# Optimization experiments

Hardware: AMD Instinct MI355X
Metric: run time of the kernel (lower is better)

Reference implementation:

```python
import jax, jax.numpy as jnp
import numpy as np
from jax.ops import segment_sum, segment_max

E = 300000
H = 256
NC = 20000
EPS = 1e-6
RESIDUAL_UNIFORM = 0.2


def setup_inputs() -> dict:
    key = jax.random.key(0)
    k = jax.random.split(key, 6)
    edge_repr = jax.random.normal(k[0], (E, H), dtype=jnp.float32)
    edge_weight = jax.random.uniform(k[1], (E,), dtype=jnp.float32)
    case_idx = jax.random.randint(k[2], (E,), 0, NC)
    W1 = jax.random.normal(k[3], (4 * H, H), dtype=jnp.float32) * (1.0 / np.sqrt(4 * H))
    b1 = jnp.zeros((H,), dtype=jnp.float32)
    W2 = jax.random.normal(k[4], (H, 1), dtype=jnp.float32) * (1.0 / np.sqrt(H))
    b2 = jnp.zeros((1,), dtype=jnp.float32)
    return {"edge_repr": edge_repr, "edge_weight": edge_weight, "case_idx": case_idx,
            "num_case": NC, "W1": W1, "b1": b1, "W2": W2, "b2": b2}


def reference(edge_repr, edge_weight, case_idx, num_case, W1, b1, W2, b2):
    # --- leave-one-out context per edge ---
    weighted = edge_repr * edge_weight[:, None]                       # [E,H]
    case_deg = segment_sum(edge_weight, case_idx, num_segments=num_case)   # [NC]
    case_sum = segment_sum(weighted, case_idx, num_segments=num_case)      # [NC,H]
    base_case_repr = case_sum / jnp.maximum(case_deg, EPS)[:, None]        # [NC,H]

    edge_case_deg = case_deg[case_idx][:, None]                       # [E,1]
    w2d = edge_weight[:, None]
    remaining = edge_case_deg - w2d
    ctx_loocv = (case_sum[case_idx] - weighted) / jnp.maximum(remaining, 1e-8)
    fallback = (remaining <= EPS).astype(edge_repr.dtype)
    ctx = fallback * base_case_repr[case_idx] + (1.0 - fallback) * ctx_loocv  # [E,H]

    # --- attention MLP on [e, ctx, e*ctx, |e-ctx|] ---
    feat = jnp.concatenate([edge_repr, ctx, edge_repr * ctx,
                            jnp.abs(edge_repr - ctx)], axis=-1)       # [E,4H]
    h = jax.nn.relu(feat @ W1 + b1)                                   # [E,H] (dropout = identity in eval)
    logits = (h @ W2 + b2)[:, 0]                                      # [E]

    # --- grouped (per-case) stable softmax ---
    gmax = segment_max(logits, case_idx, num_segments=num_case)
    gmax = jnp.where(jnp.isneginf(gmax), jnp.zeros_like(gmax), gmax)
    exp_val = jnp.exp(logits - gmax[case_idx])
    gsum = segment_sum(exp_val, case_idx, num_segments=num_case)
    alpha = exp_val / (gsum[case_idx] + 1e-8)

    uniform_alpha = edge_weight / (case_deg[case_idx] + 1e-8)
    final_alpha = (1.0 - RESIDUAL_UNIFORM) * alpha + RESIDUAL_UNIFORM * uniform_alpha

    case_repr = segment_sum(final_alpha[:, None] * edge_repr, case_idx,
                            num_segments=num_case)                    # [NC,H]
    return case_repr
```

## Files before the change

### kernel.cpp

```cpp
#include <hip/hip_runtime.h>
#include <hip/hip_bf16.h>
#include <math.h>

#define H 256
#define EPSV 1e-6f

typedef __attribute__((ext_vector_type(8))) short bf16x8;
typedef __attribute__((ext_vector_type(4))) float f32x4;
typedef __attribute__((ext_vector_type(4))) unsigned int uint4v;

static __device__ __forceinline__ unsigned short f2bf(float x){
  union { float f; unsigned u; } v; v.f = x;
  unsigned r = v.u + 0x7FFF + ((v.u >> 16) & 1);
  return (unsigned short)(r >> 16);
}
static __device__ __forceinline__ unsigned pk2(unsigned short lo, unsigned short hi){
  return (unsigned)lo | ((unsigned)hi << 16);
}

__global__ void count_kernel(const int* __restrict__ cidx, int* __restrict__ counts, int E){
  int e = blockIdx.x * blockDim.x + threadIdx.x;
  if (e < E) atomicAdd(&counts[cidx[e]], 1);
}

__global__ __launch_bounds__(1024) void scan_offsets(const int* __restrict__ counts,
                                                     int* __restrict__ offsets, int n){
  __shared__ int a[1024];
  int tid = threadIdx.x;
  int per = (n + 1023) >> 10;
  int start = tid * per;
  int end = min(start + per, n);
  int s = 0;
  for (int i = start; i < end; ++i) s += counts[i];
  a[tid] = s;
  __syncthreads();
  for (int d = 1; d < 1024; d <<= 1){
    int v = 0;
    if (tid >= d) v = a[tid - d];
    __syncthreads();
    if (tid >= d) a[tid] += v;
    __syncthreads();
  }
  int run = a[tid] - s;
  for (int i = start; i < end; ++i){ offsets[i] = run; run += counts[i]; }
  if (tid == 1023) offsets[n] = a[1023];
}

__global__ void fill_kernel(const int* __restrict__ cidx, int* __restrict__ cursor,
                            const int* __restrict__ offs, int* __restrict__ elist, int E){
  int e = blockIdx.x * blockDim.x + threadIdx.x;
  if (e < E){
    int c = cidx[e];
    int pos = atomicAdd(&cursor[c], 1);
    elist[offs[c] + pos] = e;
  }
}

__global__ __launch_bounds__(64) void sort_lists(int* __restrict__ elist,
                                                 const int* __restrict__ offs, int nc){
  int c = blockIdx.x, lane = threadIdx.x;
  int s = offs[c], e = offs[c + 1];
  int n = e - s;
  if (n <= 1) return;
  __shared__ int vals[128];
  if (n <= 128){
    int v0 = (lane < n)      ? elist[s + lane]      : 0;
    int v1 = (64 + lane < n) ? elist[s + 64 + lane] : 0;
    vals[lane] = v0; vals[64 + lane] = v1;
    __syncthreads();
    int r0 = 0, r1 = 0;
    for (int j = 0; j < n; ++j){
      int vj = vals[j];
      r0 += (vj < v0); r1 += (vj < v1);
    }
    if (lane < n)      elist[s + r0] = v0;
    if (64 + lane < n) elist[s + r1] = v1;
  } else if (lane == 0){
    for (int i = s + 1; i < e; ++i){
      int v = elist[i];
      int j = i - 1;
      while (j >= s && elist[j] > v){ elist[j + 1] = elist[j]; --j; }
      elist[j + 1] = v;
    }
  }
}

__global__ void w1_convert(const float* __restrict__ W1, unsigned short* __restrict__ w1t2s){
  int t = blockIdx.x * blockDim.x + threadIdx.x;
  int k = t >> 8, n = t & 255;
  int kg = k >> 5, klo = k & 31;
  unsigned b = (unsigned)((n & 63) * 64 + klo * 2);
  b ^= ((b >> 7) & 3u) << 4;
  size_t byteaddr = (size_t)kg * 16384 + (size_t)(n >> 6) * 4096 + b;
  w1t2s[byteaddr >> 1] = f2bf(W1[t]);
}

__global__ __launch_bounds__(64) void case_sums(const float* __restrict__ er,
                                                const float* __restrict__ ew,
                                                const int* __restrict__ elist,
                                                const int* __restrict__ offs,
                                                float* __restrict__ csum,
                                                float* __restrict__ cdeg){
  int c = blockIdx.x, lane = threadIdx.x;
  int s = offs[c], e = offs[c + 1];
  f32x4 acc = (f32x4){0.f,0.f,0.f,0.f};
  float dacc = 0.f;
  int i = s;
  for (; i + 1 < e; i += 2){
    int e1 = elist[i], e2 = elist[i + 1];
    float w1 = ew[e1], w2 = ew[e2];
    f32x4 v1 = *(const f32x4*)&er[(size_t)e1 * H + lane * 4];
    f32x4 v2 = *(const f32x4*)&er[(size_t)e2 * H + lane * 4];
    acc += v1 * w1;
    acc += v2 * w2;
    dacc += w1; dacc += w2;
  }
  if (i < e){
    int e1 = elist[i];
    float w1 = ew[e1];
    acc += (*(const f32x4*)&er[(size_t)e1 * H + lane * 4]) * w1;
    dacc += w1;
  }
  *(f32x4*)&csum[(size_t)c * H + lane * 4] = acc;
  if (lane == 0) cdeg[c] = dacc;
}

__global__ __launch_bounds__(256, 2) void fused_mlp(
    const float* __restrict__ er, const float* __restrict__ ew,
    const int* __restrict__ cidx, const float* __restrict__ cdeg,
    const float* __restrict__ csum, const unsigned short* __restrict__ w1t2s,
    const float* __restrict__ b1, const float* __restrict__ w2,
    const float* __restrict__ b2, float* __restrict__ logits, int E)
{
  __shared__ __align__(16) unsigned short featl[4 * 2048];
  __shared__ __align__(16) unsigned short Bst[2 * 8192];
  __shared__ float lpart[4][64];
  int tid = threadIdx.x;
  long e0 = (long)blockIdx.x * 64;

  int wn = tid >> 6, lane = tid & 63;
  int l15 = lane & 15, lg = lane >> 4;

  int r = tid >> 2, q = tid & 3;
  long e = e0 + r;
  bool valid = (e < (long)E);
  long ec = valid ? e : 0;
  int   cce = cidx[ec];
  float w   = valid ? ew[ec] : 0.f;
  float deg = valid ? cdeg[cce] : 1.f;
  float rem = deg - w;
  bool  fb  = (rem <= EPSV);
  float inv  = fb ? (1.0f / fmaxf(deg, EPSV)) : (1.0f / fmaxf(rem, 1e-8f));
  float wsel = fb ? 0.f : w;
  float vm   = valid ? 1.f : 0.f;
  const float* erow = er   + (size_t)ec  * H + q * 8;
  const float* srow = csum + (size_t)cce * H + q * 8;
  unsigned packoff = (unsigned)r * 32u + ((unsigned)(q ^ ((r >> 1) & 3))) * 8u;

  f32x4 acc[4][4];
  #pragma unroll
  for (int mt = 0; mt < 4; ++mt)
    #pragma unroll
    for (int nt = 0; nt < 4; ++nt) acc[mt][nt] = (f32x4){0.f,0.f,0.f,0.f};

  f32x4 xr[2], sr[2];

#define LOADQ(HH)                                                          \
  { xr[0] = *(const f32x4*)(erow + (HH) * 32);                             \
    xr[1] = *(const f32x4*)(erow + (HH) * 32 + 4);                         \
    sr[0] = *(const f32x4*)(srow + (HH) * 32);                             \
    sr[1] = *(const f32x4*)(srow + (HH) * 32 + 4); }

#define STAGE(BUF, KG)                                                     \
  { const char* gb_ = (const char*)w1t2s + ((size_t)(KG) * 16384 +         \
                      (size_t)wn * 4096 + (size_t)lane * 16);              \
    char* lb_ = (char*)Bst + ((BUF) * 16384 + wn * 4096 + lane * 16);      \
    __builtin_amdgcn_global_load_lds((const __attribute__((address_space(1))) void*)gb_,            (__attribute__((address_space(3))) void*)lb_,            16, 0, 0); \
    __builtin_amdgcn_global_load_lds((const __attribute__((address_space(1))) void*)(gb_ + 1024),   (__attribute__((address_space(3))) void*)(lb_ + 1024),   16, 0, 0); \
    __builtin_amdgcn_global_load_lds((const __attribute__((address_space(1))) void*)(gb_ + 2048),   (__attribute__((address_space(3))) void*)(lb_ + 2048),   16, 0, 0); \
    __builtin_amdgcn_global_load_lds((const __attribute__((address_space(1))) void*)(gb_ + 3072),   (__attribute__((address_space(3))) void*)(lb_ + 3072),   16, 0, 0); }

#define CLUSTER(SG, BUF)                                                   \
  { bf16x8 bfr[4];                                                         \
    _Pragma("unroll")                                                      \
    for (int nt = 0; nt < 4; ++nt){                                        \
      unsigned lcol_ = (unsigned)(nt * 16 + l15);                          \
      unsigned by_ = (BUF) * 16384u + (unsigned)wn * 4096u + lcol_ * 64u   \
                   + (((unsigned)lg ^ ((lcol_ >> 1) & 3u)) * 16u);         \
      bfr[nt] = *(const bf16x8*)((const char*)Bst + by_);                  \
    }                                                                      \
    _Pragma("unroll")                                                      \
    for (int mt = 0; mt < 4; ++mt){                                        \
      unsigned rr_ = (unsigned)(mt * 16 + l15);                            \
      unsigned le_ = ((unsigned)lg ^ ((rr_ >> 1) & 3u)) * 8u;              \
      bf16x8 afr = *(const bf16x8*)&featl[(SG) * 2048u + rr_ * 32u + le_]; \
      _Pragma("unroll")                                                    \
      for (int nt = 0; nt < 4; ++nt)                                       \
        acc[mt][nt] = __builtin_amdgcn_mfma_f32_16x16x32_bf16(afr, bfr[nt], acc[mt][nt], 0, 0, 0); \
    }                                                                      \
  }

  STAGE(0, 0)
  STAGE(1, 8)
  LOADQ(0)

  #pragma unroll 1
  for (int h = 0; h < 8; ++h){
    int hn = (h + 1) & 7;
    {
      unsigned xw[4], cw[4], pw[4], dw[4];
      #pragma unroll
      for (int d = 0; d < 4; ++d){
        float x0 = xr[d >> 1][(d & 1) * 2 + 0] * vm, x1 = xr[d >> 1][(d & 1) * 2 + 1] * vm;
        float s0 = sr[d >> 1][(d & 1) * 2 + 0] * vm, s1 = sr[d >> 1][(d & 1) * 2 + 1] * vm;
        float c0 = (s0 - wsel * x0) * inv;
        float c1 = (s1 - wsel * x1) * inv;
        xw[d] = pk2(f2bf(x0), f2bf(x1));
        cw[d] = pk2(f2bf(c0), f2bf(c1));
        pw[d] = pk2(f2bf(x0 * c0), f2bf(x1 * c1));
        dw[d] = pk2(f2bf(fabsf(x0 - c0)), f2bf(fabsf(x1 - c1)));
      }
      *(uint4v*)&featl[0 * 2048 + packoff] = (uint4v){xw[0], xw[1], xw[2], xw[3]};
      *(uint4v*)&featl[1 * 2048 + packoff] = (uint4v){cw[0], cw[1], cw[2], cw[3]};
      *(uint4v*)&featl[2 * 2048 + packoff] = (uint4v){pw[0], pw[1], pw[2], pw[3]};
      *(uint4v*)&featl[3 * 2048 + packoff] = (uint4v){dw[0], dw[1], dw[2], dw[3]};
    }
    __syncthreads();

    CLUSTER(0, 0)
    asm volatile("s_waitcnt lgkmcnt(0)" ::: "memory");
    STAGE(0, 16 + h)
    CLUSTER(1, 1)
    asm volatile("s_waitcnt lgkmcnt(0)" ::: "memory");
    STAGE(1, 24 + h)
    LOADQ(hn)
    asm volatile("s_waitcnt vmcnt(12)" ::: "memory");
    CLUSTER(2, 0)
    asm volatile("s_waitcnt lgkmcnt(0)" ::: "memory");
    STAGE(0, hn)
    asm volatile("s_waitcnt vmcnt(12)" ::: "memory");
    CLUSTER(3, 1)
    asm volatile("s_waitcnt lgkmcnt(0)" ::: "memory");
    STAGE(1, 8 + hn)
    __syncthreads();
  }
  asm volatile("" :: "v"(xr[0][0]), "v"(xr[1][0]), "v"(sr[0][0]), "v"(sr[1][0]));
#undef LOADQ
#undef STAGE
#undef CLUSTER

  float p[4][4];
  #pragma unroll
  for (int mt = 0; mt < 4; ++mt)
    #pragma unroll
    for (int j = 0; j < 4; ++j) p[mt][j] = 0.f;

  #pragma unroll
  for (int nt = 0; nt < 4; ++nt){
    int col = wn * 64 + nt * 16 + l15;
    float b1c = b1[col], w2c = w2[col];
    #pragma unroll
    for (int mt = 0; mt < 4; ++mt)
      #pragma unroll
      for (int j = 0; j < 4; ++j)
        p[mt][j] += fmaxf(acc[mt][nt][j] + b1c, 0.f) * w2c;
  }
  #pragma unroll
  for (int mask = 1; mask < 16; mask <<= 1)
    #pragma unroll
    for (int mt = 0; mt < 4; ++mt)
      #pragma unroll
      for (int j = 0; j < 4; ++j)
        p[mt][j] += __shfl_xor(p[mt][j], mask);

  if (l15 == 0){
    #pragma unroll
    for (int mt = 0; mt < 4; ++mt)
      #pragma unroll
      for (int j = 0; j < 4; ++j)
        lpart[wn][mt * 16 + lg * 4 + j] = p[mt][j];
  }
  __syncthreads();
  if (tid < 64 && e0 + tid < (long)E)
    logits[e0 + tid] = lpart[0][tid] + lpart[1][tid] + lpart[2][tid] + lpart[3][tid] + b2[0];
}

__global__ __launch_bounds__(64) void finalize(
    const float* __restrict__ er, const float* __restrict__ ew,
    const float* __restrict__ logits, const int* __restrict__ elist,
    const int* __restrict__ offs, const float* __restrict__ cdeg,
    float* __restrict__ out)
{
  int c = blockIdx.x, lane = threadIdx.x;
  int s = offs[c], e = offs[c + 1];
  int n = e - s;
  if (n == 0){
    *(f32x4*)&out[(size_t)c * H + lane * 4] = (f32x4){0.f,0.f,0.f,0.f};
    return;
  }

  float m = -INFINITY;
  for (int i = lane; i < n; i += 64) m = fmaxf(m, logits[elist[s + i]]);
  #pragma unroll
  for (int mask = 32; mask > 0; mask >>= 1) m = fmaxf(m, __shfl_xor(m, mask));

  float sm = 0.f;
  for (int i = lane; i < n; i += 64) sm += expf(logits[elist[s + i]] - m);
  #pragma unroll
  for (int mask = 32; mask > 0; mask >>= 1) sm += __shfl_xor(sm, mask);

  float gsum = sm + 1e-8f;
  float degc = cdeg[c] + 1e-8f;

  __shared__ float fa[256];
  f32x4 acc = (f32x4){0.f,0.f,0.f,0.f};
  for (int base = 0; base < n; base += 256){
    int chunk = min(n - base, 256);
    for (int i = lane; i < chunk; i += 64){
      int ed = elist[s + base + i];
      fa[i] = 0.8f * expf(logits[ed] - m) / gsum + 0.2f * ew[ed] / degc;
    }
    __syncthreads();
    int i = 0;
    for (; i + 1 < chunk; i += 2){
      int ed0 = elist[s + base + i], ed1 = elist[s + base + i + 1];
      f32x4 v0 = *(const f32x4*)&er[(size_t)ed0 * H + lane * 4];
      f32x4 v1 = *(const f32x4*)&er[(size_t)ed1 * H + lane * 4];
      acc += fa[i] * v0;
      acc += fa[i + 1] * v1;
    }
    if (i < chunk){
      int ed0 = elist[s + base + i];
      acc += fa[i] * (*(const f32x4*)&er[(size_t)ed0 * H + lane * 4]);
    }
    __syncthreads();
  }
  *(f32x4*)&out[(size_t)c * H + lane * 4] = acc;
}

extern "C" void kernel_launch(void* const* d_in, const int* in_sizes, int n_in,
                              void* d_out, int out_size, void* d_ws, size_t ws_size,
                              hipStream_t stream){
  const float* er  = (const float*)d_in[0];
  const float* ew  = (const float*)d_in[1];
  const int*   cid = (const int*)d_in[2];
  const float* W1  = (const float*)d_in[4];
  const float* b1  = (const float*)d_in[5];
  const float* W2  = (const float*)d_in[6];
  const float* b2  = (const float*)d_in[7];
  float* out = (float*)d_out;

  int E  = in_sizes[1];
  int NC = out_size / H;

  char* ws = (char*)d_ws;
  auto al = [](size_t x){ return (x + 255) & ~(size_t)255; };
  size_t o = 0;
  int* counts = (int*)(ws + o);  o = al(o + (size_t)NC * 4);
  int* cursor = (int*)(ws + o);  o = al(o + (size_t)NC * 4);
  int* offs   = (int*)(ws + o);  o = al(o + (size_t)(NC + 1) * 4);
  int* elist  = (int*)(ws + o);  o = al(o + (size_t)E * 4);
  float* cdeg = (float*)(ws + o); o = al(o + (size_t)NC * 4);
  float* csum = (float*)(ws + o); o = al(o + (size_t)NC * H * 4);
  float* logits = (float*)(ws + o); o = al(o + (size_t)E * 4);
  unsigned short* w1t2s = (unsigned short*)(ws + o); o = al(o + (size_t)1024 * H * 2);

  hipMemsetAsync(counts, 0, (size_t)NC * 4, stream);
  hipMemsetAsync(cursor, 0, (size_t)NC * 4, stream);

  count_kernel<<<(E + 255) / 256, 256, 0, stream>>>(cid, counts, E);
  scan_offsets<<<1, 1024, 0, stream>>>(counts, offs, NC);
  fill_kernel<<<(E + 255) / 256, 256, 0, stream>>>(cid, cursor, offs, elist, E);
  sort_lists<<<NC, 64, 0, stream>>>(elist, offs, NC);
  w1_convert<<<(1024 * H) / 256, 256, 0, stream>>>(W1, w1t2s);
  case_sums<<<NC, 64, 0, stream>>>(er, ew, elist, offs, csum, cdeg);
  fused_mlp<<<(E + 63) / 64, 256, 0, stream>>>(er, ew, cid, cdeg, csum, w1t2s, b1, W2, b2, logits, E);
  finalize<<<NC, 64, 0, stream>>>(er, ew, logits, elist, offs, cdeg, out);
}
```

Before: 406.4 us.

## Fold per-case sort into case_sums, use packed bf16 conversion, unroll finalize gather

The separate sort_lists kernel is merged into case_sums. Small cases are rank-sorted in LDS and the sorted indices are read straight from shared memory, which removes one launch and a global re-read of the edge list. The fused MLP now uses the hardware packed float-to-bf16 conversion instead of manual rounding, and it skips loads for invalid rows instead of multiplying them by a mask. The finalize gather loop is unrolled by four to keep more loads in flight. Sorting stays for determinism, and large cases still fall back to a serial insertion sort.

```diff
diff --git a/kernel.cpp b/kernel.cpp
--- a/kernel.cpp
+++ b/kernel.cpp
@@ -9,13 +9,14 @@
 typedef __attribute__((ext_vector_type(4))) float f32x4;
 typedef __attribute__((ext_vector_type(4))) unsigned int uint4v;
 
+static __device__ __forceinline__ unsigned pkrn(float lo, float hi){
+  __hip_bfloat162 h = __float22bfloat162_rn(make_float2(lo, hi));
+  return *reinterpret_cast<unsigned*>(&h);
+}
 static __device__ __forceinline__ unsigned short f2bf(float x){
   union { float f; unsigned u; } v; v.f = x;
   unsigned r = v.u + 0x7FFF + ((v.u >> 16) & 1);
   return (unsigned short)(r >> 16);
-}
-static __device__ __forceinline__ unsigned pk2(unsigned short lo, unsigned short hi){
-  return (unsigned)lo | ((unsigned)hi << 16);
 }
 
 __global__ void count_kernel(const int* __restrict__ cidx, int* __restrict__ counts, int E){
@@ -56,35 +57,6 @@
   }
 }
 
-__global__ __launch_bounds__(64) void sort_lists(int* __restrict__ elist,
-                                                 const int* __restrict__ offs, int nc){
-  int c = blockIdx.x, lane = threadIdx.x;
-  int s = offs[c], e = offs[c + 1];
-  int n = e - s;
-  if (n <= 1) return;
-  __shared__ int vals[128];
-  if (n <= 128){
-    int v0 = (lane < n)      ? elist[s + lane]      : 0;
-    int v1 = (64 + lane < n) ? elist[s + 64 + lane] : 0;
-    vals[lane] = v0; vals[64 + lane] = v1;
-    __syncthreads();
-    int r0 = 0, r1 = 0;
-    for (int j = 0; j < n; ++j){
-      int vj = vals[j];
-      r0 += (vj < v0); r1 += (vj < v1);
-    }
-    if (lane < n)      elist[s + r0] = v0;
-    if (64 + lane < n) elist[s + r1] = v1;
-  } else if (lane == 0){
-    for (int i = s + 1; i < e; ++i){
-      int v = elist[i];
-      int j = i - 1;
-      while (j >= s && elist[j] > v){ elist[j + 1] = elist[j]; --j; }
-      elist[j + 1] = v;
-    }
-  }
-}
-
 __global__ void w1_convert(const float* __restrict__ W1, unsigned short* __restrict__ w1t2s){
   int t = blockIdx.x * blockDim.x + threadIdx.x;
   int k = t >> 8, n = t & 255;
@@ -97,17 +69,52 @@
 
 __global__ __launch_bounds__(64) void case_sums(const float* __restrict__ er,
                                                 const float* __restrict__ ew,
-                                                const int* __restrict__ elist,
+                                                int* __restrict__ elist,
                                                 const int* __restrict__ offs,
                                                 float* __restrict__ csum,
                                                 float* __restrict__ cdeg){
   int c = blockIdx.x, lane = threadIdx.x;
   int s = offs[c], e = offs[c + 1];
+  int n = e - s;
+  __shared__ int vals[128], svals[128];
+
+  bool lds_path = (n <= 128);
+  if (lds_path && n > 1){
+    int v0 = (lane < n)      ? elist[s + lane]      : 0x7fffffff;
+    int v1 = (64 + lane < n) ? elist[s + 64 + lane] : 0x7fffffff;
+    vals[lane] = v0; vals[64 + lane] = v1;
+    __syncthreads();
+    int r0 = 0, r1 = 0;
+    for (int j = 0; j < n; ++j){
+      int vj = vals[j];
+      r0 += (vj < v0); r1 += (vj < v1);
+    }
+    if (lane < n)      svals[r0] = v0;
+    if (64 + lane < n) svals[r1] = v1;
+    __syncthreads();
+    if (lane < n)      elist[s + lane]      = svals[lane];
+    if (64 + lane < n) elist[s + 64 + lane] = svals[64 + lane];
+  } else if (lds_path && n == 1){
+    if (lane == 0) svals[0] = elist[s];
+    __syncthreads();
+  } else {
+    if (lane == 0){
+      for (int i = s + 1; i < e; ++i){
+        int v = elist[i];
+        int j = i - 1;
+        while (j >= s && elist[j] > v){ elist[j + 1] = elist[j]; --j; }
+        elist[j + 1] = v;
+      }
+    }
+    __syncthreads();
+  }
+
   f32x4 acc = (f32x4){0.f,0.f,0.f,0.f};
   float dacc = 0.f;
-  int i = s;
-  for (; i + 1 < e; i += 2){
-    int e1 = elist[i], e2 = elist[i + 1];
+  int i = 0;
+  for (; i + 1 < n; i += 2){
+    int e1 = lds_path ? svals[i]     : elist[s + i];
+    int e2 = lds_path ? svals[i + 1] : elist[s + i + 1];
     float w1 = ew[e1], w2 = ew[e2];
     f32x4 v1 = *(const f32x4*)&er[(size_t)e1 * H + lane * 4];
     f32x4 v2 = *(const f32x4*)&er[(size_t)e2 * H + lane * 4];
@@ -115,8 +122,8 @@
     acc += v2 * w2;
     dacc += w1; dacc += w2;
   }
-  if (i < e){
-    int e1 = elist[i];
+  if (i < n){
+    int e1 = lds_path ? svals[i] : elist[s + i];
     float w1 = ew[e1];
     acc += (*(const f32x4*)&er[(size_t)e1 * H + lane * 4]) * w1;
     dacc += w1;
@@ -152,7 +159,6 @@
   bool  fb  = (rem <= EPSV);
   float inv  = fb ? (1.0f / fmaxf(deg, EPSV)) : (1.0f / fmaxf(rem, 1e-8f));
   float wsel = fb ? 0.f : w;
-  float vm   = valid ? 1.f : 0.f;
   const float* erow = er   + (size_t)ec  * H + q * 8;
   const float* srow = csum + (size_t)cce * H + q * 8;
   unsigned packoff = (unsigned)r * 32u + ((unsigned)(q ^ ((r >> 1) & 3))) * 8u;
@@ -166,10 +172,15 @@
   f32x4 xr[2], sr[2];
 
 #define LOADQ(HH)                                                          \
-  { xr[0] = *(const f32x4*)(erow + (HH) * 32);                             \
+  if (valid){                                                              \
+    xr[0] = *(const f32x4*)(erow + (HH) * 32);                             \
     xr[1] = *(const f32x4*)(erow + (HH) * 32 + 4);                         \
     sr[0] = *(const f32x4*)(srow + (HH) * 32);                             \
-    sr[1] = *(const f32x4*)(srow + (HH) * 32 + 4); }
+    sr[1] = *(const f32x4*)(srow + (HH) * 32 + 4);                         \
+  } else {                                                                 \
+    xr[0] = (f32x4){0,0,0,0}; xr[1] = (f32x4){0,0,0,0};                    \
+    sr[0] = (f32x4){0,0,0,0}; sr[1] = (f32x4){0,0,0,0};                    \
+  }
 
 #define STAGE(BUF, KG)                                                     \
   { const char* gb_ = (const char*)w1t2s + ((size_t)(KG) * 16384 +         \
@@ -211,14 +222,14 @@
       unsigned xw[4], cw[4], pw[4], dw[4];
       #pragma unroll
       for (int d = 0; d < 4; ++d){
-        float x0 = xr[d >> 1][(d & 1) * 2 + 0] * vm, x1 = xr[d >> 1][(d & 1) * 2 + 1] * vm;
-        float s0 = sr[d >> 1][(d & 1) * 2 + 0] * vm, s1 = sr[d >> 1][(d & 1) * 2 + 1] * vm;
+        float x0 = xr[d >> 1][(d & 1) * 2 + 0], x1 = xr[d >> 1][(d & 1) * 2 + 1];
+        float s0 = sr[d >> 1][(d & 1) * 2 + 0], s1 = sr[d >> 1][(d & 1) * 2 + 1];
         float c0 = (s0 - wsel * x0) * inv;
         float c1 = (s1 - wsel * x1) * inv;
-        xw[d] = pk2(f2bf(x0), f2bf(x1));
-        cw[d] = pk2(f2bf(c0), f2bf(c1));
-        pw[d] = pk2(f2bf(x0 * c0), f2bf(x1 * c1));
-        dw[d] = pk2(f2bf(fabsf(x0 - c0)), f2bf(fabsf(x1 - c1)));
+        xw[d] = pkrn(x0, x1);
+        cw[d] = pkrn(c0, c1);
+        pw[d] = pkrn(x0 * c0, x1 * c1);
+        dw[d] = pkrn(fabsf(x0 - c0), fabsf(x1 - c1));
       }
       *(uint4v*)&featl[0 * 2048 + packoff] = (uint4v){xw[0], xw[1], xw[2], xw[3]};
       *(uint4v*)&featl[1 * 2048 + packoff] = (uint4v){cw[0], cw[1], cw[2], cw[3]};
@@ -322,14 +333,19 @@
     }
     __syncthreads();
     int i = 0;
-    for (; i + 1 < chunk; i += 2){
-      int ed0 = elist[s + base + i], ed1 = elist[s + base + i + 1];
+    for (; i + 3 < chunk; i += 4){
+      int ed0 = elist[s + base + i],     ed1 = elist[s + base + i + 1];
+      int ed2 = elist[s + base + i + 2], ed3 = elist[s + base + i + 3];
       f32x4 v0 = *(const f32x4*)&er[(size_t)ed0 * H + lane * 4];
       f32x4 v1 = *(const f32x4*)&er[(size_t)ed1 * H + lane * 4];
+      f32x4 v2 = *(const f32x4*)&er[(size_t)ed2 * H + lane * 4];
+      f32x4 v3 = *(const f32x4*)&er[(size_t)ed3 * H + lane * 4];
       acc += fa[i] * v0;
       acc += fa[i + 1] * v1;
-    }
-    if (i < chunk){
+      acc += fa[i + 2] * v2;
+      acc += fa[i + 3] * v3;
+    }
+    for (; i < chunk; ++i){
       int ed0 = elist[s + base + i];
       acc += fa[i] * (*(const f32x4*)&er[(size_t)ed0 * H + lane * 4]);
     }
@@ -371,7 +387,6 @@
   count_kernel<<<(E + 255) / 256, 256, 0, stream>>>(cid, counts, E);
   scan_offsets<<<1, 1024, 0, stream>>>(counts, offs, NC);
   fill_kernel<<<(E + 255) / 256, 256, 0, stream>>>(cid, cursor, offs, elist, E);
-  sort_lists<<<NC, 64, 0, stream>>>(elist, offs, NC);
   w1_convert<<<(1024 * H) / 256, 256, 0, stream>>>(W1, w1t2s);
   case_sums<<<NC, 64, 0, stream>>>(er, ew, elist, offs, csum, cdeg);
   fused_mlp<<<(E + 63) / 64, 256, 0, stream>>>(er, ew, cid, cdeg, csum, w1t2s, b1, W2, b2, logits, E);
```

After: 402.0 us. Within noise of the previous version (-1.1%).
